# Kernel tuning notes

Measured on AMD Instinct MI355X. Metric: run time of the kernel, lower is better.

The kernel has to match this reference:

```python
import jax, jax.numpy as jnp
import numpy as np

N, E, G = 100000, 1600000, 64
D, F, FE, LV, OUT = 128, 128, 3, 3, 128
EPS = 1e-5


def setup_inputs() -> dict:
    key = jax.random.key(0)
    ks = jax.random.split(key, 12)
    nrm = lambda k, s, sc: jax.random.normal(k, s, jnp.float32) * sc
    inp = {}
    inp["node_feat"] = nrm(ks[0], (N, F), 1.0)
    inp["edge_feat"] = nrm(ks[1], (E, FE), 1.0)
    inp["edge_from_idx"] = jax.random.randint(ks[2], (E,), 0, N)
    inp["edge_to_idx"] = jax.random.randint(ks[3], (E,), 0, N)
    inp["g_idx"] = jnp.sort(jax.random.randint(ks[4], (N,), 0, G))
    inp["num_graphs"] = G
    sF, sE, sD = 1/np.sqrt(F), 1/np.sqrt(FE), 1/np.sqrt(D)
    inp["w_n2l_w"] = nrm(ks[5], (F, D), sF); inp["w_n2l_b"] = jnp.zeros((D,), jnp.float32)
    inp["w_e2l_w"] = nrm(ks[6], (LV+1, FE, D), sE); inp["w_e2l_b"] = jnp.zeros((LV+1, D), jnp.float32)
    inp["conv_w"] = nrm(ks[7], (LV, D, D), sD); inp["conv_b"] = jnp.zeros((LV, D), jnp.float32)
    inp["l2_w"] = nrm(ks[8], (LV, D, D), sD); inp["l2_b"] = jnp.zeros((LV, D), jnp.float32)
    inp["msg_bn_g"] = jnp.ones((LV+1, D), jnp.float32); inp["msg_bn_b"] = jnp.zeros((LV+1, D), jnp.float32)
    inp["hid_bn_g"] = jnp.ones((LV, D), jnp.float32); inp["hid_bn_b"] = jnp.zeros((LV, D), jnp.float32)
    inp["readout_w"] = nrm(ks[9], (D, OUT), sD); inp["readout_b"] = jnp.zeros((OUT,), jnp.float32)
    return inp


def _bn(x, g, b):
    # BatchNorm1d, training mode (biased batch variance), affine
    m = jnp.mean(x, axis=0)
    v = jnp.var(x, axis=0)
    return g * (x - m) * jax.lax.rsqrt(v + EPS) + b


def reference(node_feat, edge_feat, w_n2l_w, w_n2l_b, w_e2l_w, w_e2l_b,
              conv_w, conv_b, l2_w, l2_b, msg_bn_g, msg_bn_b,
              hid_bn_g, hid_bn_b, readout_w, readout_b,
              edge_from_idx, edge_to_idx, g_idx, num_graphs):
    n_nodes = node_feat.shape[0]
    seg = lambda m: jax.ops.segment_sum(m, edge_to_idx, num_segments=n_nodes)
    # input message: node linear + scatter_add of edge linear
    msg = node_feat @ w_n2l_w + w_n2l_b + seg(edge_feat @ w_e2l_w[0] + w_e2l_b[0])
    h = _bn(jax.nn.relu(msg), msg_bn_g[0], msg_bn_b[0])  # [N, D]
    for lv in range(conv_w.shape[0]):
        # mean-field layer: aggregate neighbor states, then linear update
        node_lin = seg(h[edge_from_idx]) @ conv_w[lv] + conv_b[lv]
        e2n = seg(edge_feat @ w_e2l_w[lv + 1] + w_e2l_b[lv + 1])
        merged = _bn(jax.nn.relu(node_lin + e2n), hid_bn_g[lv], hid_bn_b[lv])
        h = _bn(jax.nn.relu(merged @ l2_w[lv] + l2_b[lv] + h),
                msg_bn_g[lv + 1], msg_bn_b[lv + 1])
    # readout: gnn_out='last', readout_agg='max', act_last=True, bn=False
    gemb = jax.ops.segment_max(h, g_idx, num_segments=num_graphs)  # [G, D]
    return jax.nn.relu(gemb @ readout_w + readout_b)
```

## Files before the change

### kernel.cpp

```cpp
#include <hip/hip_runtime.h>
#include <hip/hip_bf16.h>

#define NN 100000
#define NE 1600000
#define DD 128
#define GG 64
#define BN_EPS 1e-5f
#define NCOPY 16

typedef unsigned short u16;
using f32x4 = __attribute__((ext_vector_type(4))) float;
using s16x8 = __attribute__((ext_vector_type(8))) short;

constexpr int SCAN_B = 1024;
constexpr int NB = (NN + SCAN_B - 1) / SCAN_B;

__device__ __forceinline__ unsigned enc_f(float v) {
  unsigned u = __float_as_uint(v);
  return (u & 0x80000000u) ? ~u : (u | 0x80000000u);
}
__device__ __forceinline__ float dec_f(unsigned k) {
  unsigned u = (k & 0x80000000u) ? (k & 0x7FFFFFFFu) : ~k;
  return __uint_as_float(u);
}
__device__ __forceinline__ u16 f2b(float x) {
  __hip_bfloat16 h = __float2bfloat16(x);
  return *(u16*)&h;
}
__device__ __forceinline__ float b2f(u16 u) {
  unsigned v = ((unsigned)u) << 16;
  return __uint_as_float(v);
}
__device__ __forceinline__ float blo(unsigned v) { return __uint_as_float(v << 16); }
__device__ __forceinline__ float bhi(unsigned v) { return __uint_as_float(v & 0xFFFF0000u); }

__global__ void k_init(int* cursor, float* stats_raw, float* stats_fin,
                       unsigned* gemb_enc) {
  int i = blockIdx.x * blockDim.x + threadIdx.x;
  if (i < NN) cursor[i] = 0;
  if (i < 7 * NCOPY * 256) stats_raw[i] = 0.f;
  if (i < 4 * 256) stats_fin[i] = 0.f;
  if (i < GG*DD) gemb_enc[i] = 0x007FFFFFu;
}

__global__ void k_fill1(const int* __restrict__ to, int* cursor, int* __restrict__ tmp_pos) {
  int e = blockIdx.x * blockDim.x + threadIdx.x;
  if (e >= NE) return;
  tmp_pos[e] = atomicAdd(&cursor[to[e]], 1);
}

__global__ void k_scan1(const int* __restrict__ deg, int* row_ptr, int* bsum) {
  __shared__ int lds[SCAN_B];
  int t = threadIdx.x, i = blockIdx.x * SCAN_B + t;
  int v = (i < NN) ? deg[i] : 0;
  lds[t] = v;
  __syncthreads();
  for (int off = 1; off < SCAN_B; off <<= 1) {
    int add = (t >= off) ? lds[t - off] : 0;
    __syncthreads();
    lds[t] += add;
    __syncthreads();
  }
  if (i < NN) row_ptr[i] = lds[t] - v;
  if (t == SCAN_B - 1) bsum[blockIdx.x] = lds[t];
}

__global__ void k_scan2(const int* __restrict__ bsum, int* boff, int* row_ptr) {
  __shared__ int lds[128];
  int t = threadIdx.x;
  int v = (t < NB) ? bsum[t] : 0;
  lds[t] = v;
  __syncthreads();
  for (int off = 1; off < 128; off <<= 1) {
    int add = (t >= off) ? lds[t - off] : 0;
    __syncthreads();
    lds[t] += add;
    __syncthreads();
  }
  if (t < NB) boff[t] = lds[t] - v;
  if (t == 127) row_ptr[NN] = lds[127];
}

__global__ void k_scan3(int* row_ptr, const int* __restrict__ boff) {
  int i = blockIdx.x * blockDim.x + threadIdx.x;
  if (i >= NN) return;
  row_ptr[i] += boff[i >> 10];
}

__global__ void k_fill2(const int* __restrict__ from, const int* __restrict__ to,
                        const int* __restrict__ tmp_pos, const int* __restrict__ row_ptr,
                        int* __restrict__ csr_src, int* __restrict__ csr_eid) {
  int e = blockIdx.x * blockDim.x + threadIdx.x;
  if (e >= NE) return;
  int pos = row_ptr[to[e]] + tmp_pos[e];
  csr_src[pos] = from[e];
  csr_eid[pos] = e;
}

__global__ void k_node_ef(const float* __restrict__ ef, const int* __restrict__ row_ptr,
                          const int* __restrict__ csr_eid, float* __restrict__ agg4) {
  int grp = (blockIdx.x * 256 + threadIdx.x) >> 4;
  if (grp >= NN) return;
  int l = threadIdx.x & 15;
  int s = row_ptr[grp], e = row_ptr[grp + 1];
  float a0 = 0.f, a1 = 0.f, a2 = 0.f;
  for (int i = s + l; i < e; i += 16) {
    int eid = csr_eid[i];
    a0 += ef[(size_t)eid * 3 + 0];
    a1 += ef[(size_t)eid * 3 + 1];
    a2 += ef[(size_t)eid * 3 + 2];
  }
#pragma unroll
  for (int off = 8; off; off >>= 1) {
    a0 += __shfl_down(a0, off, 16);
    a1 += __shfl_down(a1, off, 16);
    a2 += __shfl_down(a2, off, 16);
  }
  if (l == 0)
    ((float4*)agg4)[grp] = make_float4(a0, a1, a2, (float)(e - s));
}

__global__ void k_redstat(const float* __restrict__ raw, float* __restrict__ fin) {
  int c = threadIdx.x;
  float s = 0.f;
#pragma unroll
  for (int i = 0; i < NCOPY; ++i) s += raw[i * 256 + c];
  fin[c] = s;
}

__global__ __launch_bounds__(256)
void k_gather(const u16* __restrict__ R, u16* __restrict__ out,
              const int* __restrict__ row_ptr, const int* __restrict__ csr_src,
              const float* __restrict__ stats, const float* __restrict__ g,
              const float* __restrict__ b) {
  const int wid = (blockIdx.x * 256 + threadIdx.x) >> 6;
  if (wid >= NN) return;
  const int lane = threadIdx.x & 63;
  const int s = row_ptr[wid], e = row_ptr[wid + 1];
  const unsigned* R32 = (const unsigned*)R;
  float a0 = 0.f, a1 = 0.f;
  int i = s;
  for (; i + 7 < e; i += 8) {
    int q0 = csr_src[i],     q1 = csr_src[i + 1], q2 = csr_src[i + 2], q3 = csr_src[i + 3];
    int q4 = csr_src[i + 4], q5 = csr_src[i + 5], q6 = csr_src[i + 6], q7 = csr_src[i + 7];
    unsigned w0 = R32[(size_t)q0 * 64 + lane], w1 = R32[(size_t)q1 * 64 + lane];
    unsigned w2 = R32[(size_t)q2 * 64 + lane], w3 = R32[(size_t)q3 * 64 + lane];
    unsigned w4 = R32[(size_t)q4 * 64 + lane], w5 = R32[(size_t)q5 * 64 + lane];
    unsigned w6 = R32[(size_t)q6 * 64 + lane], w7 = R32[(size_t)q7 * 64 + lane];
    a0 += blo(w0) + blo(w1) + blo(w2) + blo(w3) + blo(w4) + blo(w5) + blo(w6) + blo(w7);
    a1 += bhi(w0) + bhi(w1) + bhi(w2) + bhi(w3) + bhi(w4) + bhi(w5) + bhi(w6) + bhi(w7);
  }
  for (; i < e; ++i) {
    unsigned v = R32[(size_t)csr_src[i] * 64 + lane];
    a0 += blo(v); a1 += bhi(v);
  }
  const int d0 = lane * 2;
  float dg = (float)(e - s);
  float m0 = stats[d0] * (1.f / NN), m1 = stats[d0 + 1] * (1.f / NN);
  float v0 = stats[DD + d0] * (1.f / NN) - m0 * m0;
  float v1 = stats[DD + d0 + 1] * (1.f / NN) - m1 * m1;
  float sc0 = g[d0] * rsqrtf(v0 + BN_EPS), sc1 = g[d0 + 1] * rsqrtf(v1 + BN_EPS);
  float sh0 = b[d0] - m0 * sc0, sh1 = b[d0 + 1] - m1 * sc1;
  float r0 = sc0 * a0 + sh0 * dg;
  float r1 = sc1 * a1 + sh1 * dg;
  unsigned pk = (unsigned)f2b(r0) | ((unsigned)f2b(r1) << 16);
  ((unsigned*)out)[(size_t)wid * 64 + lane] = pk;
}

template<int MODE>
__device__ __forceinline__ void wprep_body(
    const float* __restrict__ W, const float* __restrict__ bias,
    const float* __restrict__ in_stats, const float* __restrict__ in_g,
    const float* __restrict__ in_b,
    const float* __restrict__ res_stats, const float* __restrict__ res_g,
    const float* __restrict__ res_b,
    u16* __restrict__ WT, float* __restrict__ biasP, float* __restrict__ rese) {
  __shared__ float s_s[DD], s_t[DD];
  int t = threadIdx.x;
  if (t < DD) {
    float s = 1.f, tt = 0.f;
    if (MODE == 1) {
      float s1 = 0.f, s2 = 0.f, r1 = 0.f, r2 = 0.f;
#pragma unroll
      for (int i = 0; i < NCOPY; ++i) {
        s1 += in_stats[i * 256 + t];
        s2 += in_stats[i * 256 + DD + t];
        r1 += res_stats[i * 256 + t];
        r2 += res_stats[i * 256 + DD + t];
      }
      float mean = s1 * (1.f / NN);
      float var  = s2 * (1.f / NN) - mean * mean;
      float rs = rsqrtf(var + BN_EPS);
      s = in_g[t] * rs;
      tt = in_b[t] - mean * s;
      float m2 = r1 * (1.f / NN);
      float v2 = r2 * (1.f / NN) - m2 * m2;
      float rr = rsqrtf(v2 + BN_EPS);
      float sc = res_g[t] * rr;
      rese[t] = sc;
      rese[DD + t] = res_b[t] - m2 * sc;
    }
    s_s[t] = s; s_t[t] = tt;
  }
  __syncthreads();
  for (int idx = t; idx < DD * DD; idx += 256) {
    int k = idx >> 7, n = idx & 127;
    WT[n * DD + k] = f2b(W[idx] * s_s[k]);
  }
  if (t < DD) {
    float acc = bias[t];
    if (MODE == 1)
      for (int k = 0; k < DD; ++k) acc += s_t[k] * W[k * DD + t];
    biasP[t] = acc;
  }
}

__global__ void k_wprep0(const float* __restrict__ w_n2l_w, const float* __restrict__ w_n2l_b,
                         const float* __restrict__ conv_w, const float* __restrict__ conv_b,
                         u16* wt0, float* bp0, u16* wt1, float* bp1,
                         u16* wt3, float* bp3, u16* wt5, float* bp5) {
  int blk = blockIdx.x;
  const float* W; const float* bias; u16* WT; float* biasP;
  if (blk == 0)      { W = w_n2l_w;              bias = w_n2l_b;          WT = wt0; biasP = bp0; }
  else if (blk == 1) { W = conv_w;               bias = conv_b;           WT = wt1; biasP = bp1; }
  else if (blk == 2) { W = conv_w + DD * DD;     bias = conv_b + DD;      WT = wt3; biasP = bp3; }
  else               { W = conv_w + 2 * DD * DD; bias = conv_b + 2 * DD;  WT = wt5; biasP = bp5; }
  wprep_body<0>(W, bias, nullptr, nullptr, nullptr, nullptr, nullptr, nullptr,
                WT, biasP, nullptr);
}

__global__ void k_wprep1(const float* __restrict__ W, const float* __restrict__ bias,
                         const float* __restrict__ in_stats, const float* __restrict__ in_g,
                         const float* __restrict__ in_b,
                         const float* __restrict__ res_stats, const float* __restrict__ res_g,
                         const float* __restrict__ res_b,
                         u16* WT, float* biasP, float* rese) {
  wprep_body<1>(W, bias, in_stats, in_g, in_b, res_stats, res_g, res_b, WT, biasP, rese);
}

__device__ __forceinline__ int swz_addr(int row_bytes, int xr, int g, int o) {
  return row_bytes + ((((g & 7) ^ xr) | (g & 8)) << 4) + o;
}

template<int MODE>
__global__ __launch_bounds__(256, 2)
void k_gemm(const void* __restrict__ Ain, const u16* __restrict__ WT,
            const float* __restrict__ biasP, u16* __restrict__ out,
            float* __restrict__ stats_out,
            const float* __restrict__ rese, const u16* __restrict__ resid,
            const float4* __restrict__ agg4,
            const float* __restrict__ w_e2l, const float* __restrict__ b_e2l) {
  __shared__ __align__(16) u16 lds_a[128 * 128];
  __shared__ __align__(16) u16 lds_b[128 * 128];
  __shared__ float sstats[256];
  const int tid  = threadIdx.x;
  const int lane = tid & 63;
  const int wv   = tid >> 6;
  const int row0 = blockIdx.x * 128;

  sstats[tid] = 0.f;

#pragma unroll
  for (int c = 0; c < 8; ++c) {
    int gidx = (wv * 8 + c) * 64 + lane;
    int row = gidx >> 4, gL = gidx & 15;
    int gS = (gL & 8) | ((gL & 7) ^ (row & 7));
    const u16* gsrcB = WT + (size_t)row * DD + gS * 8;
    u16* ldstB = lds_b + (size_t)(wv * 8 + c) * 512;
    __builtin_amdgcn_global_load_lds(
        (const __attribute__((address_space(1))) unsigned int*)gsrcB,
        (__attribute__((address_space(3))) unsigned int*)ldstB, 16, 0, 0);
    if (MODE != 2) {
      int arow = row0 + row; if (arow >= NN) arow = NN - 1;
      const u16* gsrcA = (const u16*)Ain + (size_t)arow * DD + gS * 8;
      u16* ldstA = lds_a + (size_t)(wv * 8 + c) * 512;
      __builtin_amdgcn_global_load_lds(
          (const __attribute__((address_space(1))) unsigned int*)gsrcA,
          (__attribute__((address_space(3))) unsigned int*)ldstA, 16, 0, 0);
    }
  }
  if (MODE == 2) {
    const float2* Af = (const float2*)Ain;
#pragma unroll
    for (int k = 0; k < 32; ++k) {
      int idx = k * 256 + tid;
      int r = idx >> 6, ln = idx & 63;
      int n = row0 + r; if (n >= NN) n = NN - 1;
      float2 v = Af[(size_t)n * 64 + ln];
      unsigned pk = (unsigned)f2b(v.x) | ((unsigned)f2b(v.y) << 16);
      int gLn = ln >> 2, oin = (ln & 3) * 4;
      int gS = (gLn & 8) | ((gLn & 7) ^ (r & 7));
      *(unsigned*)((char*)lds_a + r * 256 + gS * 16 + oin) = pk;
    }
  }
  __syncthreads();

  const int colid = lane & 15;
  const int lgrp  = lane >> 4;
  const int rowbase = wv * 32;
  const int o = (lgrp & 1) * 8;

  s16x8 afr[2][4];
#pragma unroll
  for (int rf = 0; rf < 2; ++rf) {
    int r = rowbase + rf * 16 + colid;
    int rb = r << 8, xr = r & 7;
#pragma unroll
    for (int ks = 0; ks < 4; ++ks) {
      int g0 = ks * 4 + (lgrp >> 1);
      uint2 lo = *(const uint2*)((const char*)lds_a + swz_addr(rb, xr, g0, o));
      uint2 hi = *(const uint2*)((const char*)lds_a + swz_addr(rb, xr, g0 + 2, o));
      union { unsigned u[4]; s16x8 v; } pk;
      pk.u[0] = lo.x; pk.u[1] = lo.y; pk.u[2] = hi.x; pk.u[3] = hi.y;
      afr[rf][ks] = pk.v;
    }
  }

  s16x8 aext[2];
  if (MODE != 1) {
#pragma unroll
    for (int rf = 0; rf < 2; ++rf) {
      int r = row0 + rowbase + rf * 16 + colid;
      if (r >= NN) r = NN - 1;
      float4 a4 = agg4[r];
      union { unsigned u[4]; s16x8 v; } pk;
      pk.u[0] = (lgrp == 0) ? ((unsigned)f2b(a4.x) | ((unsigned)f2b(a4.y) << 16)) : 0u;
      pk.u[1] = (lgrp == 0) ? ((unsigned)f2b(a4.z) | ((unsigned)f2b(a4.w) << 16)) : 0u;
      pk.u[2] = 0u; pk.u[3] = 0u;
      aext[rf] = pk.v;
    }
  }
  __syncthreads();

  if (MODE == 1) {
#pragma unroll
    for (int c = 0; c < 8; ++c) {
      int gidx = (wv * 8 + c) * 64 + lane;
      int row = gidx >> 4, gL = gidx & 15;
      int gS = (gL & 8) | ((gL & 7) ^ (row & 7));
      int arow = row0 + row; if (arow >= NN) arow = NN - 1;
      const u16* gsrcR = resid + (size_t)arow * DD + gS * 8;
      u16* ldstR = lds_a + (size_t)(wv * 8 + c) * 512;
      __builtin_amdgcn_global_load_lds(
          (const __attribute__((address_space(1))) unsigned int*)gsrcR,
          (__attribute__((address_space(3))) unsigned int*)ldstR, 16, 0, 0);
    }
  }

  f32x4 acc[2][8];
#pragma unroll
  for (int cf = 0; cf < 8; ++cf) {
    const int col = cf * 16 + colid;
    const float bp = biasP[col];
    acc[0][cf] = (f32x4){bp, bp, bp, bp};
    acc[1][cf] = (f32x4){bp, bp, bp, bp};
    int nb = col << 8, xn = col & 7;
#pragma unroll
    for (int ks = 0; ks < 4; ++ks) {
      int g0 = ks * 4 + (lgrp >> 1);
      uint2 lo = *(const uint2*)((const char*)lds_b + swz_addr(nb, xn, g0, o));
      uint2 hi = *(const uint2*)((const char*)lds_b + swz_addr(nb, xn, g0 + 2, o));
      union { unsigned u[4]; s16x8 v; } pk;
      pk.u[0] = lo.x; pk.u[1] = lo.y; pk.u[2] = hi.x; pk.u[3] = hi.y;
      acc[0][cf] = __builtin_amdgcn_mfma_f32_16x16x32_bf16(afr[0][ks], pk.v, acc[0][cf], 0, 0, 0);
      acc[1][cf] = __builtin_amdgcn_mfma_f32_16x16x32_bf16(afr[1][ks], pk.v, acc[1][cf], 0, 0, 0);
    }
    if (MODE != 1) {
      union { unsigned u[4]; s16x8 v; } bx;
      if (lgrp == 0) {
        float w0 = w_e2l[col], w1 = w_e2l[DD + col];
        float w2 = w_e2l[2 * DD + col], be = b_e2l[col];
        bx.u[0] = (unsigned)f2b(w0) | ((unsigned)f2b(w1) << 16);
        bx.u[1] = (unsigned)f2b(w2) | ((unsigned)f2b(be) << 16);
      } else { bx.u[0] = 0u; bx.u[1] = 0u; }
      bx.u[2] = 0u; bx.u[3] = 0u;
      acc[0][cf] = __builtin_amdgcn_mfma_f32_16x16x32_bf16(aext[0], bx.v, acc[0][cf], 0, 0, 0);
      acc[1][cf] = __builtin_amdgcn_mfma_f32_16x16x32_bf16(aext[1], bx.v, acc[1][cf], 0, 0, 0);
    }
  }
  __syncthreads();

#pragma unroll
  for (int cf = 0; cf < 8; ++cf) {
    const int col = cf * 16 + colid;
    float sc, sh;
    if (MODE == 1) { sc = rese[col]; sh = rese[DD + col]; }
    float s = 0.f, s2 = 0.f;
    int gc = col >> 3, cb = (col & 7) * 2;
#pragma unroll
    for (int rf = 0; rf < 2; ++rf)
#pragma unroll
      for (int q = 0; q < 4; ++q) {
        int rloc = rowbase + rf * 16 + lgrp * 4 + q;
        int r = row0 + rloc;
        float v = acc[rf][cf][q];
        if (MODE == 1) {
          int gsr = (gc & 8) | ((gc & 7) ^ (rloc & 7));
          u16 rv = *(const u16*)((const char*)lds_a + rloc * 256 + gsr * 16 + cb);
          v += sc * b2f(rv) + sh;
        }
        v = fmaxf(v, 0.f);
        if (r < NN) { s += v; s2 += v * v; }
        int gso = (gc & 8) | ((gc & 7) ^ (rloc & 7));
        *(u16*)((char*)lds_b + rloc * 256 + gso * 16 + cb) = f2b(v);
      }
    s  += __shfl_xor(s, 16);  s  += __shfl_xor(s, 32);
    s2 += __shfl_xor(s2, 16); s2 += __shfl_xor(s2, 32);
    if (lgrp == 0) {
      atomicAdd(&sstats[col], s);
      atomicAdd(&sstats[DD + col], s2);
    }
  }
  __syncthreads();

#pragma unroll
  for (int k = 0; k < 8; ++k) {
    int idx = k * 256 + tid;
    int r = idx >> 4, g = idx & 15;
    if (row0 + r < NN) {
      int gd = (g & 8) | ((g & 7) ^ (r & 7));
      uint4 v = *(const uint4*)((const char*)lds_b + r * 256 + g * 16);
      *(uint4*)(out + (size_t)(row0 + r) * DD + gd * 8) = v;
    }
  }
  atomicAdd(&stats_out[(blockIdx.x & (NCOPY - 1)) * 256 + tid], sstats[tid]);
}

__global__ void k_segmax(const u16* __restrict__ R, const int* __restrict__ g_idx,
                         unsigned* __restrict__ gemb_enc,
                         const float* __restrict__ stats, const float* __restrict__ g,
                         const float* __restrict__ b) {
  int t = blockIdx.x * blockDim.x + threadIdx.x;
  int d = t & (DD - 1);
  int chunk = t >> 7;
  int n0 = chunk * 8;
  if (n0 >= NN) return;
  float mean = stats[d] * (1.f / NN);
  float var  = stats[DD + d] * (1.f / NN) - mean * mean;
  float rs = rsqrtf(var + BN_EPS);
  float scale = g[d] * rs;
  float shift = b[d] - mean * scale;
  int cur = -1; float run = 0.f;
  int nend = n0 + 8; if (nend > NN) nend = NN;
  for (int n = n0; n < nend; ++n) {
    float v = scale * b2f(R[(size_t)n * DD + d]) + shift;
    int gi = g_idx[n];
    if (gi != cur) {
      if (cur >= 0) atomicMax(&gemb_enc[cur * DD + d], enc_f(run));
      cur = gi; run = v;
    } else {
      run = fmaxf(run, v);
    }
  }
  if (cur >= 0) atomicMax(&gemb_enc[cur * DD + d], enc_f(run));
}

__global__ void k_readout(const unsigned* __restrict__ gemb,
                          const float* __restrict__ W, const float* __restrict__ b,
                          float* __restrict__ out) {
  __shared__ float row[DD];
  int g = blockIdx.x, t = threadIdx.x;
  row[t] = dec_f(gemb[g * DD + t]);
  __syncthreads();
  float acc = b[t];
  for (int d = 0; d < DD; ++d) acc += row[d] * W[d * DD + t];
  out[g * DD + t] = fmaxf(acc, 0.f);
}

extern "C" void kernel_launch(void* const* d_in, const int* in_sizes, int n_in,
                              void* d_out, int out_size, void* d_ws, size_t ws_size,
                              hipStream_t stream) {
  const float* node_feat = (const float*)d_in[0];
  const float* edge_feat = (const float*)d_in[1];
  const int*   efrom     = (const int*)d_in[2];
  const int*   eto       = (const int*)d_in[3];
  const int*   g_idx     = (const int*)d_in[4];
  const float* w_n2l_w   = (const float*)d_in[6];
  const float* w_n2l_b   = (const float*)d_in[7];
  const float* w_e2l_w   = (const float*)d_in[8];
  const float* w_e2l_b   = (const float*)d_in[9];
  const float* conv_w    = (const float*)d_in[10];
  const float* conv_b    = (const float*)d_in[11];
  const float* l2_w      = (const float*)d_in[12];
  const float* l2_b      = (const float*)d_in[13];
  const float* msg_bn_g  = (const float*)d_in[14];
  const float* msg_bn_b  = (const float*)d_in[15];
  const float* hid_bn_g  = (const float*)d_in[16];
  const float* hid_bn_b  = (const float*)d_in[17];
  const float* readout_w = (const float*)d_in[18];
  const float* readout_b = (const float*)d_in[19];
  float* out = (float*)d_out;
  (void)in_sizes; (void)n_in; (void)out_size; (void)ws_size;

  char* ws = (char*)d_ws;
  size_t off = 0;
  auto alloc = [&](size_t bytes) -> void* {
    void* p = ws + off; off += (bytes + 511) & ~(size_t)511; return p;
  };
  u16*      Pb0     = (u16*)alloc((size_t)NN * DD * 2);
  u16*      Pb1     = (u16*)alloc((size_t)NN * DD * 2);
  u16*      Pb2     = (u16*)alloc((size_t)NN * DD * 2);
  float*    agg4    = (float*)alloc((size_t)NN * 4 * 4);
  int*      cursor  = (int*)alloc((size_t)NN * 4);
  int*      row_ptr = (int*)alloc((size_t)(NN + 1) * 4);
  int*      tmp_pos = (int*)alloc((size_t)NE * 4);
  int*      csr_src = (int*)alloc((size_t)NE * 4);
  int*      csr_eid = (int*)alloc((size_t)NE * 4);
  int*      bsum    = (int*)alloc((size_t)NB * 4);
  int*      boff    = (int*)alloc((size_t)NB * 4);
  float*    stats   = (float*)alloc((size_t)7 * NCOPY * 256 * 4);
  float*    statfin = (float*)alloc((size_t)4 * 256 * 4);
  unsigned* gemb    = (unsigned*)alloc((size_t)GG * DD * 4);
  u16*      wt[7];
  float*    bp[7];
  float*    re[7];
  for (int i = 0; i < 7; ++i) {
    wt[i] = (u16*)alloc((size_t)DD * DD * 2);
    bp[i] = (float*)alloc((size_t)DD * 4);
    re[i] = (float*)alloc((size_t)2 * DD * 4);
  }

  k_init<<<(NN + 255) / 256, 256, 0, stream>>>(cursor, stats, statfin, gemb);
  k_fill1<<<(NE + 255) / 256, 256, 0, stream>>>(eto, cursor, tmp_pos);
  k_scan1<<<NB, SCAN_B, 0, stream>>>(cursor, row_ptr, bsum);
  k_scan2<<<1, 128, 0, stream>>>(bsum, boff, row_ptr);
  k_scan3<<<(NN + 255) / 256, 256, 0, stream>>>(row_ptr, boff);
  k_fill2<<<(NE + 255) / 256, 256, 0, stream>>>(efrom, eto, tmp_pos, row_ptr,
                                                csr_src, csr_eid);
  k_node_ef<<<(NN * 16 + 255) / 256, 256, 0, stream>>>(edge_feat, row_ptr, csr_eid,
                                                       agg4);
  k_wprep0<<<4, 256, 0, stream>>>(w_n2l_w, w_n2l_b, conv_w, conv_b,
                                  wt[0], bp[0], wt[1], bp[1], wt[3], bp[3], wt[5], bp[5]);

  float* msg_raw[4] = { stats + 0*NCOPY*256, stats + 1*NCOPY*256,
                        stats + 2*NCOPY*256, stats + 3*NCOPY*256 };
  float* hid_raw[3] = { stats + 4*NCOPY*256, stats + 5*NCOPY*256, stats + 6*NCOPY*256 };
  float* msg_fin[4] = { statfin, statfin + 256, statfin + 512, statfin + 768 };
  const int GEMM_GRID = (NN + 127) / 128;

  k_gemm<2><<<GEMM_GRID, 256, 0, stream>>>(node_feat, wt[0], bp[0], Pb0, msg_raw[0],
      nullptr, nullptr, (const float4*)agg4, w_e2l_w + 0 * 3 * DD, w_e2l_b + 0 * DD);
  k_redstat<<<1, 256, 0, stream>>>(msg_raw[0], msg_fin[0]);

  u16* R = Pb0; u16* other = Pb1;
  for (int lv = 0; lv < 3; ++lv) {
    int wc = 1 + 2 * lv, wl = 2 + 2 * lv;
    k_gather<<<(NN * 64 + 255) / 256, 256, 0, stream>>>(R, other, row_ptr, csr_src,
        msg_fin[lv], msg_bn_g + lv * DD, msg_bn_b + lv * DD);
    k_gemm<0><<<GEMM_GRID, 256, 0, stream>>>(other, wt[wc], bp[wc], Pb2, hid_raw[lv],
        nullptr, nullptr, (const float4*)agg4,
        w_e2l_w + (size_t)(lv + 1) * 3 * DD, w_e2l_b + (lv + 1) * DD);
    k_wprep1<<<1, 256, 0, stream>>>(l2_w + (size_t)lv * DD * DD, l2_b + lv * DD,
        hid_raw[lv], hid_bn_g + lv * DD, hid_bn_b + lv * DD,
        msg_raw[lv], msg_bn_g + lv * DD, msg_bn_b + lv * DD, wt[wl], bp[wl], re[wl]);
    k_gemm<1><<<GEMM_GRID, 256, 0, stream>>>(Pb2, wt[wl], bp[wl], other, msg_raw[lv + 1],
        re[wl], R, nullptr, nullptr, nullptr);
    k_redstat<<<1, 256, 0, stream>>>(msg_raw[lv + 1], msg_fin[lv + 1]);
    u16* t = R; R = other; other = t;
  }

  k_segmax<<<(NN / 8) * DD / 256, 256, 0, stream>>>(
      R, g_idx, gemb, msg_fin[3], msg_bn_g + 3 * DD, msg_bn_b + 3 * DD);
  k_readout<<<GG, DD, 0, stream>>>(gemb, readout_w, readout_b, out);
}
```

Measured before the change: 650.1 us.

## Shrink GEMM row tile to 64 and fold residual BN into MFMA

Halves the k_gemm row tile from 128 to 64 rows per block, which cuts LDS use (one 64-row A buffer plus the weight tile) and accumulator registers so three blocks can fit per CU, and doubles the grid. In MODE 1 the residual is now reloaded into LDS and added through extra MFMAs against a diagonal scale matrix, and the residual BN shift is folded into the precomputed bias, so the scalar per-element residual loop is removed. The output is staged back through lds_a instead of a separate buffer. The trade-off is that each block reloads the full 128x128 weight tile for half as many rows, and the residual now goes through bf16 rounding of the scale.

```diff
diff --git a/kernel.cpp b/kernel.cpp
--- a/kernel.cpp
+++ b/kernel.cpp
@@ -175,10 +175,10 @@
     const float* __restrict__ res_stats, const float* __restrict__ res_g,
     const float* __restrict__ res_b,
     u16* __restrict__ WT, float* __restrict__ biasP, float* __restrict__ rese) {
-  __shared__ float s_s[DD], s_t[DD];
+  __shared__ float s_s[DD], s_t[DD], s_sh[DD];
   int t = threadIdx.x;
   if (t < DD) {
-    float s = 1.f, tt = 0.f;
+    float s = 1.f, tt = 0.f, shv = 0.f;
     if (MODE == 1) {
       float s1 = 0.f, s2 = 0.f, r1 = 0.f, r2 = 0.f;
 #pragma unroll
@@ -198,9 +198,9 @@
       float rr = rsqrtf(v2 + BN_EPS);
       float sc = res_g[t] * rr;
       rese[t] = sc;
-      rese[DD + t] = res_b[t] - m2 * sc;
-    }
-    s_s[t] = s; s_t[t] = tt;
+      shv = res_b[t] - m2 * sc;
+    }
+    s_s[t] = s; s_t[t] = tt; s_sh[t] = shv;
   }
   __syncthreads();
   for (int idx = t; idx < DD * DD; idx += 256) {
@@ -208,7 +208,7 @@
     WT[n * DD + k] = f2b(W[idx] * s_s[k]);
   }
   if (t < DD) {
-    float acc = bias[t];
+    float acc = bias[t] + s_sh[t];
     if (MODE == 1)
       for (int k = 0; k < DD; ++k) acc += s_t[k] * W[k * DD + t];
     biasP[t] = acc;
@@ -243,20 +243,20 @@
 }
 
 template<int MODE>
-__global__ __launch_bounds__(256, 2)
+__global__ __launch_bounds__(256, 3)
 void k_gemm(const void* __restrict__ Ain, const u16* __restrict__ WT,
             const float* __restrict__ biasP, u16* __restrict__ out,
             float* __restrict__ stats_out,
             const float* __restrict__ rese, const u16* __restrict__ resid,
             const float4* __restrict__ agg4,
             const float* __restrict__ w_e2l, const float* __restrict__ b_e2l) {
-  __shared__ __align__(16) u16 lds_a[128 * 128];
-  __shared__ __align__(16) u16 lds_b[128 * 128];
+  __shared__ __align__(16) u16 lds_w[128 * 128];
+  __shared__ __align__(16) u16 lds_a[64 * 128];
   __shared__ float sstats[256];
   const int tid  = threadIdx.x;
   const int lane = tid & 63;
   const int wv   = tid >> 6;
-  const int row0 = blockIdx.x * 128;
+  const int row0 = blockIdx.x * 64;
 
   sstats[tid] = 0.f;
 
@@ -266,44 +266,48 @@
     int row = gidx >> 4, gL = gidx & 15;
     int gS = (gL & 8) | ((gL & 7) ^ (row & 7));
     const u16* gsrcB = WT + (size_t)row * DD + gS * 8;
-    u16* ldstB = lds_b + (size_t)(wv * 8 + c) * 512;
+    u16* ldstB = lds_w + (size_t)(wv * 8 + c) * 512;
     __builtin_amdgcn_global_load_lds(
         (const __attribute__((address_space(1))) unsigned int*)gsrcB,
         (__attribute__((address_space(3))) unsigned int*)ldstB, 16, 0, 0);
-    if (MODE != 2) {
+  }
+  if (MODE != 2) {
+#pragma unroll
+    for (int c = 0; c < 4; ++c) {
+      int gidx = (wv * 4 + c) * 64 + lane;
+      int row = gidx >> 4, gL = gidx & 15;
+      int gS = (gL & 8) | ((gL & 7) ^ (row & 7));
       int arow = row0 + row; if (arow >= NN) arow = NN - 1;
       const u16* gsrcA = (const u16*)Ain + (size_t)arow * DD + gS * 8;
-      u16* ldstA = lds_a + (size_t)(wv * 8 + c) * 512;
+      u16* ldstA = lds_a + (size_t)(wv * 4 + c) * 512;
       __builtin_amdgcn_global_load_lds(
           (const __attribute__((address_space(1))) unsigned int*)gsrcA,
           (__attribute__((address_space(3))) unsigned int*)ldstA, 16, 0, 0);
     }
-  }
-  if (MODE == 2) {
+  } else {
     const float2* Af = (const float2*)Ain;
 #pragma unroll
-    for (int k = 0; k < 32; ++k) {
-      int idx = k * 256 + tid;
-      int r = idx >> 6, ln = idx & 63;
-      int n = row0 + r; if (n >= NN) n = NN - 1;
+    for (int k = 0; k < 16; ++k) {
+      int idx = k * 64 + lane;
+      int rloc = wv * 16 + (idx >> 6);
+      int ln = idx & 63;
+      int n = row0 + rloc; if (n >= NN) n = NN - 1;
       float2 v = Af[(size_t)n * 64 + ln];
       unsigned pk = (unsigned)f2b(v.x) | ((unsigned)f2b(v.y) << 16);
       int gLn = ln >> 2, oin = (ln & 3) * 4;
-      int gS = (gLn & 8) | ((gLn & 7) ^ (r & 7));
-      *(unsigned*)((char*)lds_a + r * 256 + gS * 16 + oin) = pk;
+      int gS = (gLn & 8) | ((gLn & 7) ^ (rloc & 7));
+      *(unsigned*)((char*)lds_a + rloc * 256 + gS * 16 + oin) = pk;
     }
   }
   __syncthreads();
 
   const int colid = lane & 15;
   const int lgrp  = lane >> 4;
-  const int rowbase = wv * 32;
   const int o = (lgrp & 1) * 8;
 
-  s16x8 afr[2][4];
-#pragma unroll
-  for (int rf = 0; rf < 2; ++rf) {
-    int r = rowbase + rf * 16 + colid;
+  s16x8 afr[4];
+  {
+    int r = wv * 16 + colid;
     int rb = r << 8, xr = r & 7;
 #pragma unroll
     for (int ks = 0; ks < 4; ++ks) {
@@ -312,58 +316,52 @@
       uint2 hi = *(const uint2*)((const char*)lds_a + swz_addr(rb, xr, g0 + 2, o));
       union { unsigned u[4]; s16x8 v; } pk;
       pk.u[0] = lo.x; pk.u[1] = lo.y; pk.u[2] = hi.x; pk.u[3] = hi.y;
-      afr[rf][ks] = pk.v;
-    }
-  }
-
-  s16x8 aext[2];
+      afr[ks] = pk.v;
+    }
+  }
+
+  s16x8 aext;
   if (MODE != 1) {
-#pragma unroll
-    for (int rf = 0; rf < 2; ++rf) {
-      int r = row0 + rowbase + rf * 16 + colid;
-      if (r >= NN) r = NN - 1;
-      float4 a4 = agg4[r];
-      union { unsigned u[4]; s16x8 v; } pk;
-      pk.u[0] = (lgrp == 0) ? ((unsigned)f2b(a4.x) | ((unsigned)f2b(a4.y) << 16)) : 0u;
-      pk.u[1] = (lgrp == 0) ? ((unsigned)f2b(a4.z) | ((unsigned)f2b(a4.w) << 16)) : 0u;
-      pk.u[2] = 0u; pk.u[3] = 0u;
-      aext[rf] = pk.v;
-    }
-  }
-  __syncthreads();
+    int r = row0 + wv * 16 + colid;
+    if (r >= NN) r = NN - 1;
+    float4 a4 = agg4[r];
+    union { unsigned u[4]; s16x8 v; } pk;
+    pk.u[0] = (lgrp == 0) ? ((unsigned)f2b(a4.x) | ((unsigned)f2b(a4.y) << 16)) : 0u;
+    pk.u[1] = (lgrp == 0) ? ((unsigned)f2b(a4.z) | ((unsigned)f2b(a4.w) << 16)) : 0u;
+    pk.u[2] = 0u; pk.u[3] = 0u;
+    aext = pk.v;
+  }
 
   if (MODE == 1) {
 #pragma unroll
-    for (int c = 0; c < 8; ++c) {
-      int gidx = (wv * 8 + c) * 64 + lane;
+    for (int c = 0; c < 4; ++c) {
+      int gidx = (wv * 4 + c) * 64 + lane;
       int row = gidx >> 4, gL = gidx & 15;
       int gS = (gL & 8) | ((gL & 7) ^ (row & 7));
       int arow = row0 + row; if (arow >= NN) arow = NN - 1;
       const u16* gsrcR = resid + (size_t)arow * DD + gS * 8;
-      u16* ldstR = lds_a + (size_t)(wv * 8 + c) * 512;
+      u16* ldstR = lds_a + (size_t)(wv * 4 + c) * 512;
       __builtin_amdgcn_global_load_lds(
           (const __attribute__((address_space(1))) unsigned int*)gsrcR,
           (__attribute__((address_space(3))) unsigned int*)ldstR, 16, 0, 0);
     }
   }
 
-  f32x4 acc[2][8];
+  f32x4 acc[8];
 #pragma unroll
   for (int cf = 0; cf < 8; ++cf) {
     const int col = cf * 16 + colid;
     const float bp = biasP[col];
-    acc[0][cf] = (f32x4){bp, bp, bp, bp};
-    acc[1][cf] = (f32x4){bp, bp, bp, bp};
+    acc[cf] = (f32x4){bp, bp, bp, bp};
     int nb = col << 8, xn = col & 7;
 #pragma unroll
     for (int ks = 0; ks < 4; ++ks) {
       int g0 = ks * 4 + (lgrp >> 1);
-      uint2 lo = *(const uint2*)((const char*)lds_b + swz_addr(nb, xn, g0, o));
-      uint2 hi = *(const uint2*)((const char*)lds_b + swz_addr(nb, xn, g0 + 2, o));
+      uint2 lo = *(const uint2*)((const char*)lds_w + swz_addr(nb, xn, g0, o));
+      uint2 hi = *(const uint2*)((const char*)lds_w + swz_addr(nb, xn, g0 + 2, o));
       union { unsigned u[4]; s16x8 v; } pk;
       pk.u[0] = lo.x; pk.u[1] = lo.y; pk.u[2] = hi.x; pk.u[3] = hi.y;
-      acc[0][cf] = __builtin_amdgcn_mfma_f32_16x16x32_bf16(afr[0][ks], pk.v, acc[0][cf], 0, 0, 0);
-      acc[1][cf] = __builtin_amdgcn_mfma_f32_16x16x32_bf16(afr[1][ks], pk.v, acc[1][cf], 0, 0, 0);
+      acc[cf] = __builtin_amdgcn_mfma_f32_16x16x32_bf16(afr[ks], pk.v, acc[cf], 0, 0, 0);
     }
     if (MODE != 1) {
       union { unsigned u[4]; s16x8 v; } bx;
@@ -374,36 +372,54 @@
         bx.u[1] = (unsigned)f2b(w2) | ((unsigned)f2b(be) << 16);
       } else { bx.u[0] = 0u; bx.u[1] = 0u; }
       bx.u[2] = 0u; bx.u[3] = 0u;
-      acc[0][cf] = __builtin_amdgcn_mfma_f32_16x16x32_bf16(aext[0], bx.v, acc[0][cf], 0, 0, 0);
-      acc[1][cf] = __builtin_amdgcn_mfma_f32_16x16x32_bf16(aext[1], bx.v, acc[1][cf], 0, 0, 0);
-    }
-  }
-  __syncthreads();
+      acc[cf] = __builtin_amdgcn_mfma_f32_16x16x32_bf16(aext, bx.v, acc[cf], 0, 0, 0);
+    }
+  }
+
+  if (MODE == 1) {
+    __syncthreads();
+    s16x8 afrR[4];
+    {
+      int r = wv * 16 + colid;
+      int rb = r << 8, xr = r & 7;
+#pragma unroll
+      for (int ks = 0; ks < 4; ++ks) {
+        int g0 = ks * 4 + (lgrp >> 1);
+        uint2 lo = *(const uint2*)((const char*)lds_a + swz_addr(rb, xr, g0, o));
+        uint2 hi = *(const uint2*)((const char*)lds_a + swz_addr(rb, xr, g0 + 2, o));
+        union { unsigned u[4]; s16x8 v; } pk;
+        pk.u[0] = lo.x; pk.u[1] = lo.y; pk.u[2] = hi.x; pk.u[3] = hi.y;
+        afrR[ks] = pk.v;
+      }
+    }
+#pragma unroll
+    for (int cf = 0; cf < 8; ++cf) {
+      const int col = cf * 16 + colid;
+      union { unsigned u[4]; s16x8 v; } bx;
+      bx.u[0] = 0u; bx.u[1] = 0u; bx.u[2] = 0u; bx.u[3] = 0u;
+      if (lgrp == (colid >> 2)) {
+        float scv = rese[col];
+        int j = (colid & 3) + 4 * (cf & 1);
+        bx.u[j >> 1] = ((unsigned)f2b(scv)) << (16 * (j & 1));
+      }
+      acc[cf] = __builtin_amdgcn_mfma_f32_16x16x32_bf16(afrR[cf >> 1], bx.v, acc[cf], 0, 0, 0);
+    }
+  }
 
 #pragma unroll
   for (int cf = 0; cf < 8; ++cf) {
     const int col = cf * 16 + colid;
-    float sc, sh;
-    if (MODE == 1) { sc = rese[col]; sh = rese[DD + col]; }
     float s = 0.f, s2 = 0.f;
     int gc = col >> 3, cb = (col & 7) * 2;
 #pragma unroll
-    for (int rf = 0; rf < 2; ++rf)
-#pragma unroll
-      for (int q = 0; q < 4; ++q) {
-        int rloc = rowbase + rf * 16 + lgrp * 4 + q;
-        int r = row0 + rloc;
-        float v = acc[rf][cf][q];
-        if (MODE == 1) {
-          int gsr = (gc & 8) | ((gc & 7) ^ (rloc & 7));
-          u16 rv = *(const u16*)((const char*)lds_a + rloc * 256 + gsr * 16 + cb);
-          v += sc * b2f(rv) + sh;
-        }
-        v = fmaxf(v, 0.f);
-        if (r < NN) { s += v; s2 += v * v; }
-        int gso = (gc & 8) | ((gc & 7) ^ (rloc & 7));
-        *(u16*)((char*)lds_b + rloc * 256 + gso * 16 + cb) = f2b(v);
-      }
+    for (int q = 0; q < 4; ++q) {
+      int rloc = wv * 16 + lgrp * 4 + q;
+      int r = row0 + rloc;
+      float v = fmaxf(acc[cf][q], 0.f);
+      if (r < NN) { s += v; s2 += v * v; }
+      int gso = (gc & 8) | ((gc & 7) ^ (rloc & 7));
+      *(u16*)((char*)lds_a + rloc * 256 + gso * 16 + cb) = f2b(v);
+    }
     s  += __shfl_xor(s, 16);  s  += __shfl_xor(s, 32);
     s2 += __shfl_xor(s2, 16); s2 += __shfl_xor(s2, 32);
     if (lgrp == 0) {
@@ -414,13 +430,13 @@
   __syncthreads();
 
 #pragma unroll
-  for (int k = 0; k < 8; ++k) {
-    int idx = k * 256 + tid;
-    int r = idx >> 4, g = idx & 15;
-    if (row0 + r < NN) {
-      int gd = (g & 8) | ((g & 7) ^ (r & 7));
-      uint4 v = *(const uint4*)((const char*)lds_b + r * 256 + g * 16);
-      *(uint4*)(out + (size_t)(row0 + r) * DD + gd * 8) = v;
+  for (int k = 0; k < 4; ++k) {
+    int idx = k * 64 + lane;
+    int rloc = wv * 16 + (idx >> 4), g = idx & 15;
+    if (row0 + rloc < NN) {
+      int gd = (g & 8) | ((g & 7) ^ (rloc & 7));
+      uint4 v = *(const uint4*)((const char*)lds_a + rloc * 256 + g * 16);
+      *(uint4*)(out + (size_t)(row0 + rloc) * DD + gd * 8) = v;
     }
   }
   atomicAdd(&stats_out[(blockIdx.x & (NCOPY - 1)) * 256 + tid], sstats[tid]);
@@ -536,7 +552,7 @@
                         stats + 2*NCOPY*256, stats + 3*NCOPY*256 };
   float* hid_raw[3] = { stats + 4*NCOPY*256, stats + 5*NCOPY*256, stats + 6*NCOPY*256 };
   float* msg_fin[4] = { statfin, statfin + 256, statfin + 512, statfin + 768 };
-  const int GEMM_GRID = (NN + 127) / 128;
+  const int GEMM_GRID = (NN + 63) / 64;
 
   k_gemm<2><<<GEMM_GRID, 256, 0, stream>>>(node_feat, wt[0], bp[0], Pb0, msg_raw[0],
       nullptr, nullptr, (const float4*)agg4, w_e2l_w + 0 * 3 * DD, w_e2l_b + 0 * DD);
```

Result: slower. 752.9 us (+15.8%).

## Interleave CSR src/eid arrays and gather four edges per wave with 16-byte loads

Applied to the files above, without the earlier changes.

Merges the separate csr_src and csr_eid arrays into one interleaved uint2 array. The gather kernel is restructured so each wave covers four neighbor rows at once, 16 lanes per row, each lane loading a uint4 (8 bf16 values). Partial sums are then combined across quarter-waves with xor shuffles. This cuts the number of load instructions and raises bytes per request. The cost is that the CSR index reads now move 8 bytes per edge instead of 4, and only a quarter of the lanes do the final normalize-and-store.

```diff
diff --git a/kernel.cpp b/kernel.cpp
--- a/kernel.cpp
+++ b/kernel.cpp
@@ -89,23 +89,22 @@
 
 __global__ void k_fill2(const int* __restrict__ from, const int* __restrict__ to,
                         const int* __restrict__ tmp_pos, const int* __restrict__ row_ptr,
-                        int* __restrict__ csr_src, int* __restrict__ csr_eid) {
+                        uint2* __restrict__ csr2) {
   int e = blockIdx.x * blockDim.x + threadIdx.x;
   if (e >= NE) return;
   int pos = row_ptr[to[e]] + tmp_pos[e];
-  csr_src[pos] = from[e];
-  csr_eid[pos] = e;
+  csr2[pos] = make_uint2((unsigned)from[e], (unsigned)e);
 }
 
 __global__ void k_node_ef(const float* __restrict__ ef, const int* __restrict__ row_ptr,
-                          const int* __restrict__ csr_eid, float* __restrict__ agg4) {
+                          const uint2* __restrict__ csr2, float* __restrict__ agg4) {
   int grp = (blockIdx.x * 256 + threadIdx.x) >> 4;
   if (grp >= NN) return;
   int l = threadIdx.x & 15;
   int s = row_ptr[grp], e = row_ptr[grp + 1];
   float a0 = 0.f, a1 = 0.f, a2 = 0.f;
   for (int i = s + l; i < e; i += 16) {
-    int eid = csr_eid[i];
+    int eid = (int)csr2[i].y;
     a0 += ef[(size_t)eid * 3 + 0];
     a1 += ef[(size_t)eid * 3 + 1];
     a2 += ef[(size_t)eid * 3 + 2];
@@ -130,41 +129,74 @@
 
 __global__ __launch_bounds__(256)
 void k_gather(const u16* __restrict__ R, u16* __restrict__ out,
-              const int* __restrict__ row_ptr, const int* __restrict__ csr_src,
+              const int* __restrict__ row_ptr, const uint2* __restrict__ csr2,
               const float* __restrict__ stats, const float* __restrict__ g,
               const float* __restrict__ b) {
   const int wid = (blockIdx.x * 256 + threadIdx.x) >> 6;
   if (wid >= NN) return;
   const int lane = threadIdx.x & 63;
+  const int esel = lane >> 4;
+  const int dpos = lane & 15;
   const int s = row_ptr[wid], e = row_ptr[wid + 1];
-  const unsigned* R32 = (const unsigned*)R;
-  float a0 = 0.f, a1 = 0.f;
+  const uint4* R4 = (const uint4*)R;
+  float a0 = 0.f, a1 = 0.f, a2 = 0.f, a3 = 0.f;
+  float a4 = 0.f, a5 = 0.f, a6 = 0.f, a7 = 0.f;
+#define ACC(V)                                                       \
+  a0 += blo(V.x); a1 += bhi(V.x); a2 += blo(V.y); a3 += bhi(V.y);    \
+  a4 += blo(V.z); a5 += bhi(V.z); a6 += blo(V.w); a7 += bhi(V.w);
   int i = s;
-  for (; i + 7 < e; i += 8) {
-    int q0 = csr_src[i],     q1 = csr_src[i + 1], q2 = csr_src[i + 2], q3 = csr_src[i + 3];
-    int q4 = csr_src[i + 4], q5 = csr_src[i + 5], q6 = csr_src[i + 6], q7 = csr_src[i + 7];
-    unsigned w0 = R32[(size_t)q0 * 64 + lane], w1 = R32[(size_t)q1 * 64 + lane];
-    unsigned w2 = R32[(size_t)q2 * 64 + lane], w3 = R32[(size_t)q3 * 64 + lane];
-    unsigned w4 = R32[(size_t)q4 * 64 + lane], w5 = R32[(size_t)q5 * 64 + lane];
-    unsigned w6 = R32[(size_t)q6 * 64 + lane], w7 = R32[(size_t)q7 * 64 + lane];
-    a0 += blo(w0) + blo(w1) + blo(w2) + blo(w3) + blo(w4) + blo(w5) + blo(w6) + blo(w7);
-    a1 += bhi(w0) + bhi(w1) + bhi(w2) + bhi(w3) + bhi(w4) + bhi(w5) + bhi(w6) + bhi(w7);
-  }
-  for (; i < e; ++i) {
-    unsigned v = R32[(size_t)csr_src[i] * 64 + lane];
-    a0 += blo(v); a1 += bhi(v);
-  }
-  const int d0 = lane * 2;
-  float dg = (float)(e - s);
-  float m0 = stats[d0] * (1.f / NN), m1 = stats[d0 + 1] * (1.f / NN);
-  float v0 = stats[DD + d0] * (1.f / NN) - m0 * m0;
-  float v1 = stats[DD + d0 + 1] * (1.f / NN) - m1 * m1;
-  float sc0 = g[d0] * rsqrtf(v0 + BN_EPS), sc1 = g[d0 + 1] * rsqrtf(v1 + BN_EPS);
-  float sh0 = b[d0] - m0 * sc0, sh1 = b[d0 + 1] - m1 * sc1;
-  float r0 = sc0 * a0 + sh0 * dg;
-  float r1 = sc1 * a1 + sh1 * dg;
-  unsigned pk = (unsigned)f2b(r0) | ((unsigned)f2b(r1) << 16);
-  ((unsigned*)out)[(size_t)wid * 64 + lane] = pk;
+  for (; i + 15 < e; i += 16) {
+    int q0 = (int)csr2[i      + esel].x;
+    int q1 = (int)csr2[i + 4  + esel].x;
+    int q2 = (int)csr2[i + 8  + esel].x;
+    int q3 = (int)csr2[i + 12 + esel].x;
+    uint4 w0 = R4[(size_t)q0 * 16 + dpos];
+    uint4 w1 = R4[(size_t)q1 * 16 + dpos];
+    uint4 w2 = R4[(size_t)q2 * 16 + dpos];
+    uint4 w3 = R4[(size_t)q3 * 16 + dpos];
+    ACC(w0) ACC(w1) ACC(w2) ACC(w3)
+  }
+  for (; i + 3 < e; i += 4) {
+    int q = (int)csr2[i + esel].x;
+    uint4 wv = R4[(size_t)q * 16 + dpos];
+    ACC(wv)
+  }
+  if (i < e && esel < e - i) {
+    int q = (int)csr2[i + esel].x;
+    uint4 wv = R4[(size_t)q * 16 + dpos];
+    ACC(wv)
+  }
+#undef ACC
+  a0 += __shfl_xor(a0, 16); a1 += __shfl_xor(a1, 16);
+  a2 += __shfl_xor(a2, 16); a3 += __shfl_xor(a3, 16);
+  a4 += __shfl_xor(a4, 16); a5 += __shfl_xor(a5, 16);
+  a6 += __shfl_xor(a6, 16); a7 += __shfl_xor(a7, 16);
+  a0 += __shfl_xor(a0, 32); a1 += __shfl_xor(a1, 32);
+  a2 += __shfl_xor(a2, 32); a3 += __shfl_xor(a3, 32);
+  a4 += __shfl_xor(a4, 32); a5 += __shfl_xor(a5, 32);
+  a6 += __shfl_xor(a6, 32); a7 += __shfl_xor(a7, 32);
+  if (esel == 0) {
+    const int d0 = dpos * 8;
+    float dg = (float)(e - s);
+    float a[8] = {a0, a1, a2, a3, a4, a5, a6, a7};
+    unsigned pk[4];
+#pragma unroll
+    for (int h = 0; h < 4; ++h) {
+      float r[2];
+#pragma unroll
+      for (int j = 0; j < 2; ++j) {
+        int d = d0 + h * 2 + j;
+        float m  = stats[d] * (1.f / NN);
+        float vv = stats[DD + d] * (1.f / NN) - m * m;
+        float sc = g[d] * rsqrtf(vv + BN_EPS);
+        float sh = b[d] - m * sc;
+        r[j] = sc * a[h * 2 + j] + sh * dg;
+      }
+      pk[h] = (unsigned)f2b(r[0]) | ((unsigned)f2b(r[1]) << 16);
+    }
+    uint4 v; v.x = pk[0]; v.y = pk[1]; v.z = pk[2]; v.w = pk[3];
+    ((uint4*)out)[(size_t)wid * 16 + dpos] = v;
+  }
 }
 
 template<int MODE>
@@ -504,8 +536,7 @@
   int*      cursor  = (int*)alloc((size_t)NN * 4);
   int*      row_ptr = (int*)alloc((size_t)(NN + 1) * 4);
   int*      tmp_pos = (int*)alloc((size_t)NE * 4);
-  int*      csr_src = (int*)alloc((size_t)NE * 4);
-  int*      csr_eid = (int*)alloc((size_t)NE * 4);
+  uint2*    csr2    = (uint2*)alloc((size_t)NE * 8);
   int*      bsum    = (int*)alloc((size_t)NB * 4);
   int*      boff    = (int*)alloc((size_t)NB * 4);
   float*    stats   = (float*)alloc((size_t)7 * NCOPY * 256 * 4);
@@ -525,9 +556,8 @@
   k_scan1<<<NB, SCAN_B, 0, stream>>>(cursor, row_ptr, bsum);
   k_scan2<<<1, 128, 0, stream>>>(bsum, boff, row_ptr);
   k_scan3<<<(NN + 255) / 256, 256, 0, stream>>>(row_ptr, boff);
-  k_fill2<<<(NE + 255) / 256, 256, 0, stream>>>(efrom, eto, tmp_pos, row_ptr,
-                                                csr_src, csr_eid);
-  k_node_ef<<<(NN * 16 + 255) / 256, 256, 0, stream>>>(edge_feat, row_ptr, csr_eid,
+  k_fill2<<<(NE + 255) / 256, 256, 0, stream>>>(efrom, eto, tmp_pos, row_ptr, csr2);
+  k_node_ef<<<(NN * 16 + 255) / 256, 256, 0, stream>>>(edge_feat, row_ptr, csr2,
                                                        agg4);
   k_wprep0<<<4, 256, 0, stream>>>(w_n2l_w, w_n2l_b, conv_w, conv_b,
                                   wt[0], bp[0], wt[1], bp[1], wt[3], bp[3], wt[5], bp[5]);
@@ -545,7 +575,7 @@
   u16* R = Pb0; u16* other = Pb1;
   for (int lv = 0; lv < 3; ++lv) {
     int wc = 1 + 2 * lv, wl = 2 + 2 * lv;
-    k_gather<<<(NN * 64 + 255) / 256, 256, 0, stream>>>(R, other, row_ptr, csr_src,
+    k_gather<<<(NN * 64 + 255) / 256, 256, 0, stream>>>(R, other, row_ptr, csr2,
         msg_fin[lv], msg_bn_g + lv * DD, msg_bn_b + lv * DD);
     k_gemm<0><<<GEMM_GRID, 256, 0, stream>>>(other, wt[wc], bp[wc], Pb2, hid_raw[lv],
         nullptr, nullptr, (const float4*)agg4,
```

Result: faster. 602.9 us (-7.3%).
